# Kernel tuning notes

Measured on AMD Instinct MI355X. Metric: run time of the kernel, lower is better.

Reference implementation:

```python
import jax, jax.numpy as jnp
import numpy as np

N, E, IN_DIM, HID, G, NCLS, LAYERS = 200000, 1200000, 128, 64, 1024, 6, 3
BN_EPS = 1e-5


def _bn(x, g, b, m, v):
    # eval-mode BatchNorm1d with running stats
    return (x - m) * jax.lax.rsqrt(v + BN_EPS) * g + b


def setup_inputs() -> dict:
    key = jax.random.key(0)
    ks = jax.random.split(key, 24)
    s = 0.05
    d = {
        "x": jax.random.normal(ks[0], (N, IN_DIM), jnp.float32),
        "edge_index": jax.random.randint(ks[1], (2, E), 0, N, dtype=jnp.int32),
        "batch": jnp.sort(jax.random.randint(ks[2], (N,), 0, G, dtype=jnp.int32)),
        # input embedding + input BN
        "emb_w": jax.random.normal(ks[3], (IN_DIM, HID), jnp.float32) * s,
        "emb_b": jnp.zeros((HID,), jnp.float32),
        "ibn_g": jnp.ones((HID,), jnp.float32),
        "ibn_b": jnp.zeros((HID,), jnp.float32),
        "ibn_m": jax.random.normal(ks[4], (HID,), jnp.float32) * 0.1,
        "ibn_v": jax.random.uniform(ks[5], (HID,), jnp.float32, 0.5, 1.5),
        # stacked per-layer GIN MLP params [LAYERS, ...]
        "fc1_w": jax.random.normal(ks[6], (LAYERS, HID, HID), jnp.float32) * s,
        "fc1_b": jnp.zeros((LAYERS, HID), jnp.float32),
        "mbn_g": jnp.ones((LAYERS, HID), jnp.float32),
        "mbn_b": jnp.zeros((LAYERS, HID), jnp.float32),
        "mbn_m": jax.random.normal(ks[7], (LAYERS, HID), jnp.float32) * 0.1,
        "mbn_v": jax.random.uniform(ks[8], (LAYERS, HID), jnp.float32, 0.5, 1.5),
        "fc2_w": jax.random.normal(ks[9], (LAYERS, HID, HID), jnp.float32) * s,
        "fc2_b": jnp.zeros((LAYERS, HID), jnp.float32),
        # stacked per-layer outer BN params
        "obn_g": jnp.ones((LAYERS, HID), jnp.float32),
        "obn_b": jnp.zeros((LAYERS, HID), jnp.float32),
        "obn_m": jax.random.normal(ks[10], (LAYERS, HID), jnp.float32) * 0.1,
        "obn_v": jax.random.uniform(ks[11], (LAYERS, HID), jnp.float32, 0.5, 1.5),
        # classifier head
        "cls1_w": jax.random.normal(ks[12], (HID, HID // 2), jnp.float32) * s,
        "cls1_b": jnp.zeros((HID // 2,), jnp.float32),
        "cls2_w": jax.random.normal(ks[13], (HID // 2, NCLS), jnp.float32) * s,
        "cls2_b": jnp.zeros((NCLS,), jnp.float32),
    }
    return d


def reference(x, edge_index, batch,
              emb_w, emb_b, ibn_g, ibn_b, ibn_m, ibn_v,
              fc1_w, fc1_b, mbn_g, mbn_b, mbn_m, mbn_v, fc2_w, fc2_b,
              obn_g, obn_b, obn_m, obn_v,
              cls1_w, cls1_b, cls2_w, cls2_b):
    n = x.shape[0]
    src, dst = edge_index[0], edge_index[1]

    # input embed -> BN -> relu (dropout = identity in eval)
    h = jnp.dot(x, emb_w) + emb_b
    h = jax.nn.relu(_bn(h, ibn_g, ibn_b, ibn_m, ibn_v))

    for i in range(LAYERS):
        # GINConv (eps=0): aggregate neighbors via scatter-add, then MLP
        agg = jax.ops.segment_sum(h[src], dst, num_segments=n)
        z = h + agg
        z = jnp.dot(z, fc1_w[i]) + fc1_b[i]
        z = jax.nn.relu(_bn(z, mbn_g[i], mbn_b[i], mbn_m[i], mbn_v[i]))
        z = jnp.dot(z, fc2_w[i]) + fc2_b[i]
        # outer BN + relu
        h = jax.nn.relu(_bn(z, obn_g[i], obn_b[i], obn_m[i], obn_v[i]))

    # global mean pool per graph
    sums = jax.ops.segment_sum(h, batch, num_segments=G)
    cnts = jax.ops.segment_sum(jnp.ones((n,), h.dtype), batch, num_segments=G)
    pooled = sums / jnp.maximum(cnts, 1.0)[:, None]

    # classifier
    out = jax.nn.relu(jnp.dot(pooled, cls1_w) + cls1_b)
    out = jnp.dot(out, cls2_w) + cls2_b
    return out
```

## Files before the change

### kernel.cpp

```cpp
#include <hip/hip_runtime.h>
#include <hip/hip_bf16.h>

#define N_NODES 200000
#define N_EDGES 1200000
#define IN_DIM  128
#define HID     64
#define NGRAPH  1024
#define NCLS    6
#define BN_EPS  1e-5f

#define TILE_N   64
#define ZS       68
#define ECAP     1024

#define SCAN_CHUNK 1024
#define NBLK_SCAN ((N_NODES + SCAN_CHUNK - 1) / SCAN_CHUNK)

#define NBKT   128
#define BRANGE 1568
#define BCAP   12288
#define EPB    4096
#define NB_BIN ((N_EDGES + EPB - 1) / EPB)

typedef short bf16x8 __attribute__((ext_vector_type(8)));
typedef float f32x4  __attribute__((ext_vector_type(4)));
#define MFMA16(a,b,c) __builtin_amdgcn_mfma_f32_16x16x32_bf16((a),(b),(c),0,0,0)

__device__ __forceinline__ unsigned short f2bf(float f) {
    union { __hip_bfloat16 h; unsigned short u; } v; v.h = __float2bfloat16(f); return v.u;
}
__device__ __forceinline__ float bfbits2f(unsigned short u) {
    union { unsigned int i; float f; } v; v.i = ((unsigned int)u) << 16; return v.f;
}
__device__ __forceinline__ void cvt4(const float4& x, uint2& hi, uint2& lo) {
    const unsigned short h0 = f2bf(x.x), h1 = f2bf(x.y), h2 = f2bf(x.z), h3 = f2bf(x.w);
    hi.x = (unsigned)h0 | ((unsigned)h1 << 16);
    hi.y = (unsigned)h2 | ((unsigned)h3 << 16);
    const unsigned short l0 = f2bf(x.x - bfbits2f(h0)), l1 = f2bf(x.y - bfbits2f(h1));
    const unsigned short l2 = f2bf(x.z - bfbits2f(h2)), l3 = f2bf(x.w - bfbits2f(h3));
    lo.x = (unsigned)l0 | ((unsigned)l1 << 16);
    lo.y = (unsigned)l2 | ((unsigned)l3 << 16);
}

__global__ __launch_bounds__(256) void prep_emb_kernel(
    const float* __restrict__ w, unsigned short* __restrict__ wpe)
{
    const int idx = blockIdx.x * 256 + threadIdx.x;
    if (idx >= 16384) return;
    const int j = idx & 7, l = (idx >> 3) & 63;
    const int plane = (idx >> 9) & 1, s = (idx >> 10) & 3, ct = (idx >> 12) & 3;
    const int n = ct * 16 + (l & 15);
    const int k = s * 32 + (l >> 4) * 8 + j;
    const float f = w[k * 64 + n];
    const unsigned short hb = f2bf(f);
    wpe[idx] = plane ? f2bf(f - bfbits2f(hb)) : hb;
}

__global__ __launch_bounds__(256) void prep_fc_kernel(
    const float* __restrict__ fc1, const float* __restrict__ fc2,
    unsigned short* __restrict__ wpf)
{
    const int idx = blockIdx.x * 256 + threadIdx.x;
    if (idx >= 49152) return;
    const int j = idx & 7, l = (idx >> 3) & 63;
    const int plane = (idx >> 9) & 1, s = (idx >> 10) & 1, ct = (idx >> 11) & 3;
    const int g = (idx >> 13) & 1, layer = idx >> 14;
    const int n = ct * 16 + (l & 15);
    const int k = s * 32 + (l >> 4) * 8 + j;
    const float* W = g ? fc2 : fc1;
    const float f = W[(layer * 64 + k) * 64 + n];
    const unsigned short hb = f2bf(f);
    wpf[idx] = plane ? f2bf(f - bfbits2f(hb)) : hb;
}

__global__ __launch_bounds__(256) void bin_kernel(
    const int* __restrict__ src, const int* __restrict__ dst,
    int* __restrict__ gcnt, uint2* __restrict__ ebin)
{
    __shared__ int hist[NBKT];
    __shared__ int basis[NBKT];
    const int t = threadIdx.x;
    const int base = blockIdx.x * EPB;
    if (t < NBKT) hist[t] = 0;
    __syncthreads();
    int sv[16], dv[16];
    #pragma unroll
    for (int i = 0; i < 16; i++) {
        const int e = base + t + i * 256;
        if (e < N_EDGES) {
            sv[i] = src[e]; dv[i] = dst[e];
            atomicAdd(&hist[dv[i] / BRANGE], 1);
        } else { sv[i] = -1; dv[i] = -1; }
    }
    __syncthreads();
    if (t < NBKT) { basis[t] = atomicAdd(&gcnt[t], hist[t]); hist[t] = 0; }
    __syncthreads();
    #pragma unroll
    for (int i = 0; i < 16; i++) {
        if (dv[i] >= 0) {
            const int bb = dv[i] / BRANGE;
            const int pos = basis[bb] + atomicAdd(&hist[bb], 1);
            ebin[(size_t)bb * BCAP + pos] = make_uint2((unsigned)sv[i], (unsigned)dv[i]);
        }
    }
}

__global__ __launch_bounds__(512) void bindeg_kernel(
    const int* __restrict__ gcnt, const uint2* __restrict__ ebin,
    int* __restrict__ deg)
{
    __shared__ int hist[BRANGE];
    const int b = blockIdx.x, t = threadIdx.x;
    for (int i = t; i < BRANGE; i += 512) hist[i] = 0;
    __syncthreads();
    const int cnt = gcnt[b];
    const int r0 = b * BRANGE;
    const uint2* __restrict__ eb = ebin + (size_t)b * BCAP;
    for (int i = t; i < cnt; i += 512)
        atomicAdd(&hist[(int)eb[i].y - r0], 1);
    __syncthreads();
    for (int i = t; i < BRANGE; i += 512)
        if (r0 + i < N_NODES) deg[r0 + i] = hist[i];
}

__global__ __launch_bounds__(512) void binscatter_kernel(
    const int* __restrict__ gcnt, const uint2* __restrict__ ebin,
    const int* __restrict__ offs, int* __restrict__ csr_src)
{
    __shared__ int cur[BRANGE];
    const int b = blockIdx.x, t = threadIdx.x;
    const int r0 = b * BRANGE;
    const int lim = (r0 + BRANGE <= N_NODES) ? BRANGE : (N_NODES - r0);
    for (int i = t; i < lim; i += 512) cur[i] = offs[r0 + i];
    __syncthreads();
    const int cnt = gcnt[b];
    const uint2* __restrict__ eb = ebin + (size_t)b * BCAP;
    for (int i = t; i < cnt; i += 512) {
        const uint2 e = eb[i];
        const int pos = atomicAdd(&cur[(int)e.y - r0], 1);
        csr_src[pos] = (int)e.x;
    }
}

__global__ __launch_bounds__(256) void scan_sum_kernel(
    const int* __restrict__ deg, int* __restrict__ bsum)
{
    __shared__ int sd[256];
    const int b = blockIdx.x, t = threadIdx.x;
    const int base = b * SCAN_CHUNK;
    int s = 0;
    #pragma unroll
    for (int i = 0; i < SCAN_CHUNK / 256; i++) {
        const int idx = base + t + i * 256;
        s += (idx < N_NODES) ? deg[idx] : 0;
    }
    sd[t] = s; __syncthreads();
    for (int off = 128; off > 0; off >>= 1) {
        if (t < off) sd[t] += sd[t + off];
        __syncthreads();
    }
    if (t == 0) bsum[b] = sd[0];
}

__global__ __launch_bounds__(256) void scan_block_kernel(
    const int* __restrict__ bsum, int* __restrict__ boff, int* __restrict__ offs)
{
    __shared__ int sd[256];
    const int t = threadIdx.x;
    const int v = (t < NBLK_SCAN) ? bsum[t] : 0;
    sd[t] = v; __syncthreads();
    for (int off = 1; off < 256; off <<= 1) {
        const int u = (t >= off) ? sd[t - off] : 0;
        __syncthreads();
        sd[t] += u;
        __syncthreads();
    }
    if (t < NBLK_SCAN) boff[t] = sd[t] - v;
    if (t == 0) offs[N_NODES] = N_EDGES;
}

__global__ __launch_bounds__(256) void scan_scatter_kernel(
    const int* __restrict__ deg, const int* __restrict__ boff, int* __restrict__ offs)
{
    __shared__ int sd[256];
    const int b = blockIdx.x, t = threadIdx.x;
    const int base = b * SCAN_CHUNK + t * 4;
    int d0 = 0, d1 = 0, d2 = 0, d3 = 0;
    if (base + 0 < N_NODES) d0 = deg[base + 0];
    if (base + 1 < N_NODES) d1 = deg[base + 1];
    if (base + 2 < N_NODES) d2 = deg[base + 2];
    if (base + 3 < N_NODES) d3 = deg[base + 3];
    const int ts = d0 + d1 + d2 + d3;
    sd[t] = ts; __syncthreads();
    for (int off = 1; off < 256; off <<= 1) {
        const int u = (t >= off) ? sd[t - off] : 0;
        __syncthreads();
        sd[t] += u;
        __syncthreads();
    }
    const int excl = sd[t] - ts + boff[b];
    if (base + 0 < N_NODES) offs[base + 0] = excl;
    if (base + 1 < N_NODES) offs[base + 1] = excl + d0;
    if (base + 2 < N_NODES) offs[base + 2] = excl + d0 + d1;
    if (base + 3 < N_NODES) offs[base + 3] = excl + d0 + d1 + d2;
}

__global__ __launch_bounds__(256) void graph_offs_kernel(
    const int* __restrict__ batch, int* __restrict__ goffs)
{
    const int g = blockIdx.x * 256 + threadIdx.x;
    if (g > NGRAPH) return;
    if (g == NGRAPH) { goffs[NGRAPH] = N_NODES; return; }
    int lo = 0, hi = N_NODES;
    while (lo < hi) {
        const int mid = (lo + hi) >> 1;
        if (batch[mid] < g) lo = mid + 1; else hi = mid;
    }
    goffs[g] = lo;
}

__global__ __launch_bounds__(256) void pool_kernel(
    const float* __restrict__ h, const int* __restrict__ goffs,
    float* __restrict__ pooled, float* __restrict__ cnt)
{
    __shared__ float4 red[4][16];
    const int g = blockIdx.x, t = threadIdx.x;
    const int s = goffs[g], e = goffs[g + 1];
    const int grp = t >> 4;
    const int q = t & 15;
    float4 acc = {0.f, 0.f, 0.f, 0.f};
    for (int n = s + grp; n < e; n += 16) {
        const float4 v = *(const float4*)(h + (size_t)n * HID + q * 4);
        acc.x += v.x; acc.y += v.y; acc.z += v.z; acc.w += v.w;
    }
    #pragma unroll
    for (int off = 16; off <= 32; off <<= 1) {
        acc.x += __shfl_xor(acc.x, off, 64);
        acc.y += __shfl_xor(acc.y, off, 64);
        acc.z += __shfl_xor(acc.z, off, 64);
        acc.w += __shfl_xor(acc.w, off, 64);
    }
    const int wv = t >> 6, lane = t & 63;
    if (lane < 16) red[wv][lane] = acc;
    __syncthreads();
    if (t < 16) {
        float4 a = red[0][t];
        const float4 b = red[1][t], c = red[2][t], d = red[3][t];
        a.x += b.x + c.x + d.x;
        a.y += b.y + c.y + d.y;
        a.z += b.z + c.z + d.z;
        a.w += b.w + c.w + d.w;
        *(float4*)(pooled + (size_t)g * HID + t * 4) = a;
    }
    if (t == 0) cnt[g] = (float)(e - s);
}

__global__ __launch_bounds__(256) void embed_kernel(
    const float* __restrict__ x, const unsigned short* __restrict__ wpe,
    const float* __restrict__ bias,
    const float* __restrict__ bn_g, const float* __restrict__ bn_b,
    const float* __restrict__ bn_m, const float* __restrict__ bn_v,
    float* __restrict__ h)
{
    __shared__ __align__(16) short Abuf[4 * 4 * 2 * 64 * 8];
    __shared__ float Ztmp[TILE_N * ZS];
    __shared__ float BNs[128];
    const int t = threadIdx.x, lane = t & 63, w = t >> 6;
    const int base = blockIdx.x * TILE_N;

    if (t < 64) {
        const float s = bn_g[t] * rsqrtf(bn_v[t] + BN_EPS);
        BNs[t] = s;
        BNs[64 + t] = bias[t] * s + bn_b[t] - bn_m[t] * s;
    }
    #pragma unroll
    for (int i = 0; i < 8; i++) {
        const int idx = t + i * 256;
        const int n = idx >> 5, k4 = idx & 31;
        const float4 v = *(const float4*)(x + (size_t)(base + n) * IN_DIM + k4 * 4);
        uint2 hi, lo; cvt4(v, hi, lo);
        const int s = k4 >> 3, lc = (n & 15) + 16 * ((k4 >> 1) & 3);
        const int half = k4 & 1, wm = n >> 4;
        *(uint2*)&Abuf[(((wm * 4 + s) * 2 + 0) * 64 + lc) * 8 + half * 4] = hi;
        *(uint2*)&Abuf[(((wm * 4 + s) * 2 + 1) * 64 + lc) * 8 + half * 4] = lo;
    }
    __syncthreads();

    const bf16x8* A = (const bf16x8*)Abuf;
    const bf16x8* B = (const bf16x8*)wpe;
    bf16x8 ah[4], al[4];
    #pragma unroll
    for (int s = 0; s < 4; s++) {
        ah[s] = A[((w * 4 + s) * 2 + 0) * 64 + lane];
        al[s] = A[((w * 4 + s) * 2 + 1) * 64 + lane];
    }
    const int q = lane >> 4, c = lane & 15;
    #pragma unroll
    for (int ct = 0; ct < 4; ct++) {
        f32x4 acc = {0.f, 0.f, 0.f, 0.f};
        #pragma unroll
        for (int s = 0; s < 4; s++) {
            const bf16x8 bh = B[(ct << 9) + (s << 7) + lane];
            const bf16x8 bl = B[(ct << 9) + (s << 7) + 64 + lane];
            acc = MFMA16(ah[s], bh, acc);
            acc = MFMA16(ah[s], bl, acc);
            acc = MFMA16(al[s], bh, acc);
        }
        const int n = ct * 16 + c;
        const float sc = BNs[n], sh = BNs[64 + n];
        #pragma unroll
        for (int r = 0; r < 4; r++)
            Ztmp[(w * 16 + q * 4 + r) * ZS + n] = fmaxf(acc[r] * sc + sh, 0.f);
    }
    __syncthreads();
    #pragma unroll
    for (int i = 0; i < 4; i++) {
        const int idx = t + i * 256, n = idx >> 4, k4 = idx & 15;
        *(float4*)(h + (size_t)(base + n) * HID + k4 * 4) =
            *(const float4*)(&Ztmp[n * ZS + k4 * 4]);
    }
}

__global__ __launch_bounds__(256) void agg_mlp_kernel(
    const float* __restrict__ hin, float* __restrict__ hout,
    const int* __restrict__ offs, const int* __restrict__ csr,
    const unsigned short* __restrict__ wp1, const unsigned short* __restrict__ wp2,
    const float* __restrict__ b1, const float* __restrict__ g1,
    const float* __restrict__ bb1, const float* __restrict__ m1, const float* __restrict__ v1,
    const float* __restrict__ b2, const float* __restrict__ g2,
    const float* __restrict__ bb2, const float* __restrict__ m2, const float* __restrict__ v2)
{
    __shared__ __align__(16) short Abuf[4 * 2 * 2 * 64 * 8];
    __shared__ float Ztmp[TILE_N * ZS];
    __shared__ int   OF[TILE_N + 1];
    __shared__ int   EIDX[ECAP];
    __shared__ float BNs[256];
    const int t = threadIdx.x, lane = t & 63, w = t >> 6;
    const int sub = lane >> 4, cq = lane & 15;
    const int base = blockIdx.x * TILE_N;

    if (t < 64) {
        const float sa = g1[t] * rsqrtf(v1[t] + BN_EPS);
        BNs[t] = sa; BNs[64 + t] = b1[t] * sa + bb1[t] - m1[t] * sa;
        const float sb = g2[t] * rsqrtf(v2[t] + BN_EPS);
        BNs[128 + t] = sb; BNs[192 + t] = b2[t] * sb + bb2[t] - m2[t] * sb;
    }
    if (t <= TILE_N) OF[t] = offs[base + t];
    const int segStart = offs[base];
    const int segEnd   = offs[base + TILE_N];
    for (int i = t; i < segEnd - segStart; i += 256)
        if (i < ECAP) EIDX[i] = csr[segStart + i];
    __syncthreads();

    const float* __restrict__ hc = hin + cq * 4;
    #pragma unroll
    for (int p = 0; p < 4; p++) {
        const int mloc = p * 4 + sub, nl = w * 16 + mloc;
        const int e0 = OF[nl], e1 = OF[nl + 1];
        float4 acc = *(const float4*)(hin + (size_t)(base + nl) * HID + cq * 4);
        if (e0 < e1) {
            const int e1m = e1 - 1;
            for (int e = e0; e < e1; e += 4) {
                const int ea = e;
                const int eb = (e + 1 < e1) ? e + 1 : e1m;
                const int ec = (e + 2 < e1) ? e + 2 : e1m;
                const int ed = (e + 3 < e1) ? e + 3 : e1m;
                const int la = ea - segStart, lb = eb - segStart;
                const int lc2 = ec - segStart, ld = ed - segStart;
                const int s0 = (la < ECAP) ? EIDX[la] : csr[ea];
                const int s1 = (lb < ECAP) ? EIDX[lb] : csr[eb];
                const int s2 = (lc2 < ECAP) ? EIDX[lc2] : csr[ec];
                const int s3 = (ld < ECAP) ? EIDX[ld] : csr[ed];
                const float4 v0 = *(const float4*)(hc + (size_t)s0 * HID);
                const float4 v1_ = *(const float4*)(hc + (size_t)s1 * HID);
                const float4 v2_ = *(const float4*)(hc + (size_t)s2 * HID);
                const float4 v3_ = *(const float4*)(hc + (size_t)s3 * HID);
                const float mk1 = (e + 1 < e1) ? 1.f : 0.f;
                const float mk2 = (e + 2 < e1) ? 1.f : 0.f;
                const float mk3 = (e + 3 < e1) ? 1.f : 0.f;
                acc.x += v0.x + mk1 * v1_.x + mk2 * v2_.x + mk3 * v3_.x;
                acc.y += v0.y + mk1 * v1_.y + mk2 * v2_.y + mk3 * v3_.y;
                acc.z += v0.z + mk1 * v1_.z + mk2 * v2_.z + mk3 * v3_.z;
                acc.w += v0.w + mk1 * v1_.w + mk2 * v2_.w + mk3 * v3_.w;
            }
        }
        uint2 hi, lo; cvt4(acc, hi, lo);
        const int s = cq >> 3, lc = mloc + 16 * ((cq >> 1) & 3), half = cq & 1;
        *(uint2*)&Abuf[(((w * 2 + s) * 2 + 0) * 64 + lc) * 8 + half * 4] = hi;
        *(uint2*)&Abuf[(((w * 2 + s) * 2 + 1) * 64 + lc) * 8 + half * 4] = lo;
    }
    __syncthreads();

    const bf16x8* A = (const bf16x8*)Abuf;
    const int q = lane >> 4, c = lane & 15;

    {
        const bf16x8 a0h = A[((w * 2 + 0) * 2 + 0) * 64 + lane];
        const bf16x8 a0l = A[((w * 2 + 0) * 2 + 1) * 64 + lane];
        const bf16x8 a1h = A[((w * 2 + 1) * 2 + 0) * 64 + lane];
        const bf16x8 a1l = A[((w * 2 + 1) * 2 + 1) * 64 + lane];
        const bf16x8* B = (const bf16x8*)wp1;
        #pragma unroll
        for (int ct = 0; ct < 4; ct++) {
            const bf16x8 b0h = B[(ct << 8) + lane];
            const bf16x8 b0l = B[(ct << 8) + 64 + lane];
            const bf16x8 b1h_ = B[(ct << 8) + 128 + lane];
            const bf16x8 b1l_ = B[(ct << 8) + 192 + lane];
            f32x4 acc = {0.f, 0.f, 0.f, 0.f};
            acc = MFMA16(a0h, b0h, acc);
            acc = MFMA16(a0h, b0l, acc);
            acc = MFMA16(a0l, b0h, acc);
            acc = MFMA16(a1h, b1h_, acc);
            acc = MFMA16(a1h, b1l_, acc);
            acc = MFMA16(a1l, b1h_, acc);
            const int n = ct * 16 + c;
            const float sc = BNs[n], sh = BNs[64 + n];
            #pragma unroll
            for (int r = 0; r < 4; r++)
                Ztmp[(w * 16 + q * 4 + r) * ZS + n] = fmaxf(acc[r] * sc + sh, 0.f);
        }
    }
    __syncthreads();

    {
        const int m = t >> 2;
        #pragma unroll
        for (int d = 0; d < 4; d++) {
            const int k4 = (t & 3) * 4 + d;
            const float4 v = *(const float4*)(&Ztmp[m * ZS + k4 * 4]);
            uint2 hi, lo; cvt4(v, hi, lo);
            const int s = k4 >> 3, lc = (m & 15) + 16 * ((k4 >> 1) & 3);
            const int half = k4 & 1, wm = m >> 4;
            *(uint2*)&Abuf[(((wm * 2 + s) * 2 + 0) * 64 + lc) * 8 + half * 4] = hi;
            *(uint2*)&Abuf[(((wm * 2 + s) * 2 + 1) * 64 + lc) * 8 + half * 4] = lo;
        }
    }
    __syncthreads();

    {
        const bf16x8 a0h = A[((w * 2 + 0) * 2 + 0) * 64 + lane];
        const bf16x8 a0l = A[((w * 2 + 0) * 2 + 1) * 64 + lane];
        const bf16x8 a1h = A[((w * 2 + 1) * 2 + 0) * 64 + lane];
        const bf16x8 a1l = A[((w * 2 + 1) * 2 + 1) * 64 + lane];
        const bf16x8* B = (const bf16x8*)wp2;
        #pragma unroll
        for (int ct = 0; ct < 4; ct++) {
            const bf16x8 b0h = B[(ct << 8) + lane];
            const bf16x8 b0l = B[(ct << 8) + 64 + lane];
            const bf16x8 b1h_ = B[(ct << 8) + 128 + lane];
            const bf16x8 b1l_ = B[(ct << 8) + 192 + lane];
            f32x4 acc = {0.f, 0.f, 0.f, 0.f};
            acc = MFMA16(a0h, b0h, acc);
            acc = MFMA16(a0h, b0l, acc);
            acc = MFMA16(a0l, b0h, acc);
            acc = MFMA16(a1h, b1h_, acc);
            acc = MFMA16(a1h, b1l_, acc);
            acc = MFMA16(a1l, b1h_, acc);
            const int n = ct * 16 + c;
            const float sc = BNs[128 + n], sh = BNs[192 + n];
            #pragma unroll
            for (int r = 0; r < 4; r++)
                Ztmp[(w * 16 + q * 4 + r) * ZS + n] = fmaxf(acc[r] * sc + sh, 0.f);
        }
    }
    __syncthreads();

    #pragma unroll
    for (int i = 0; i < 4; i++) {
        const int idx = t + i * 256, n = idx >> 4, k4 = idx & 15;
        *(float4*)(hout + (size_t)(base + n) * HID + k4 * 4) =
            *(const float4*)(&Ztmp[n * ZS + k4 * 4]);
    }
}

__global__ __launch_bounds__(64) void cls_kernel(
    const float* __restrict__ pooled, const float* __restrict__ cnt,
    const float* __restrict__ w1, const float* __restrict__ b1,
    const float* __restrict__ w2, const float* __restrict__ b2,
    float* __restrict__ out)
{
    const int g = blockIdx.x;
    const int lane = threadIdx.x;
    const float c = cnt[g];
    const float p = pooled[(size_t)g * HID + lane] / fmaxf(c, 1.f);
    float acc = (lane < 32) ? b1[lane] : 0.f;
    #pragma unroll
    for (int k = 0; k < 64; k++) {
        const float pk = __shfl(p, k, 64);
        if (lane < 32) acc += pk * w1[k * 32 + lane];
    }
    const float hmid = fmaxf(acc, 0.f);
    float acc2 = (lane < NCLS) ? b2[lane] : 0.f;
    #pragma unroll
    for (int k = 0; k < 32; k++) {
        const float hk = __shfl(hmid, k, 64);
        if (lane < NCLS) acc2 += hk * w2[k * NCLS + lane];
    }
    if (lane < NCLS) out[(size_t)g * NCLS + lane] = acc2;
}

extern "C" void kernel_launch(void* const* d_in, const int* in_sizes, int n_in,
                              void* d_out, int out_size, void* d_ws, size_t ws_size,
                              hipStream_t stream) {
    const float* x     = (const float*)d_in[0];
    const int*   ei    = (const int*)d_in[1];
    const int*   batch = (const int*)d_in[2];
    const float* emb_w = (const float*)d_in[3];
    const float* emb_b = (const float*)d_in[4];
    const float* ibn_g = (const float*)d_in[5];
    const float* ibn_b = (const float*)d_in[6];
    const float* ibn_m = (const float*)d_in[7];
    const float* ibn_v = (const float*)d_in[8];
    const float* fc1_w = (const float*)d_in[9];
    const float* fc1_b = (const float*)d_in[10];
    const float* mbn_g = (const float*)d_in[11];
    const float* mbn_b = (const float*)d_in[12];
    const float* mbn_m = (const float*)d_in[13];
    const float* mbn_v = (const float*)d_in[14];
    const float* fc2_w = (const float*)d_in[15];
    const float* fc2_b = (const float*)d_in[16];
    const float* obn_g = (const float*)d_in[17];
    const float* obn_b = (const float*)d_in[18];
    const float* obn_m = (const float*)d_in[19];
    const float* obn_v = (const float*)d_in[20];
    const float* cls1w = (const float*)d_in[21];
    const float* cls1b = (const float*)d_in[22];
    const float* cls2w = (const float*)d_in[23];
    const float* cls2b = (const float*)d_in[24];

    float* h0     = (float*)d_ws;
    float* h1     = h0 + (size_t)N_NODES * HID;
    float* pooled = h1 + (size_t)N_NODES * HID;
    float* cnt    = pooled + NGRAPH * HID;
    int*   deg    = (int*)(cnt + NGRAPH);
    int*   offs   = deg + N_NODES;
    int*   bsum   = offs + (N_NODES + 1);
    int*   boff   = bsum + NBLK_SCAN;
    int*   csr    = boff + NBLK_SCAN;
    unsigned short* wpe = (unsigned short*)(csr + N_EDGES);
    unsigned short* wpf = wpe + 16384;
    int*   goffs  = (int*)(wpf + 49152);
    int*   gcnt   = goffs + (NGRAPH + 1);
    uint2* ebin   = (uint2*)h0;

    const int* src = ei;
    const int* dst = ei + N_EDGES;

    prep_emb_kernel<<<64, 256, 0, stream>>>(emb_w, wpe);
    prep_fc_kernel<<<192, 256, 0, stream>>>(fc1_w, fc2_w, wpf);

    graph_offs_kernel<<<(NGRAPH + 256) / 256, 256, 0, stream>>>(batch, goffs);

    hipMemsetAsync(gcnt, 0, NBKT * sizeof(int), stream);
    bin_kernel<<<NB_BIN, 256, 0, stream>>>(src, dst, gcnt, ebin);
    bindeg_kernel<<<NBKT, 512, 0, stream>>>(gcnt, ebin, deg);
    scan_sum_kernel<<<NBLK_SCAN, 256, 0, stream>>>(deg, bsum);
    scan_block_kernel<<<1, 256, 0, stream>>>(bsum, boff, offs);
    scan_scatter_kernel<<<NBLK_SCAN, 256, 0, stream>>>(deg, boff, offs);
    binscatter_kernel<<<NBKT, 512, 0, stream>>>(gcnt, ebin, offs, csr);

    const int gemm_blocks = N_NODES / TILE_N;
    embed_kernel<<<gemm_blocks, 256, 0, stream>>>(x, wpe, emb_b,
                                                  ibn_g, ibn_b, ibn_m, ibn_v, h0);

    const float* hin = h0;
    float* hout = h1;
    for (int i = 0; i < 3; i++) {
        agg_mlp_kernel<<<gemm_blocks, 256, 0, stream>>>(
            hin, hout, offs, csr,
            wpf + (size_t)(i * 2 + 0) * 8192, wpf + (size_t)(i * 2 + 1) * 8192,
            fc1_b + i * HID, mbn_g + i * HID, mbn_b + i * HID, mbn_m + i * HID, mbn_v + i * HID,
            fc2_b + i * HID, obn_g + i * HID, obn_b + i * HID, obn_m + i * HID, obn_v + i * HID);
        const float* tmp = hin; hin = hout; hout = (float*)tmp;
    }

    pool_kernel<<<NGRAPH, 256, 0, stream>>>(h1, goffs, pooled, cnt);

    cls_kernel<<<NGRAPH, 64, 0, stream>>>(pooled, cnt, cls1w, cls1b, cls2w, cls2b,
                                          (float*)d_out);
}
```

Measured before the change: 526.9 us.

## Alias A-fragment and Z staging buffers in LDS, swizzle slots, raise occupancy

The bf16 A-fragment buffer and the fp32 Ztmp staging tile now share one LDS allocation in both the embed and agg/MLP kernels, with extra barriers so each phase finishes reading before the next overwrites it. An XOR swizzle is applied to the 16-byte fragment slot index to spread LDS bank accesses. agg_mlp_kernel gets a launch_bounds occupancy hint of 7 blocks. The aim is lower LDS use and more resident blocks for the latency-bound gather, at the cost of additional __syncthreads and possible register-pressure spills.

```diff
diff --git a/kernel.cpp b/kernel.cpp
--- a/kernel.cpp
+++ b/kernel.cpp
@@ -21,6 +21,8 @@
 #define BCAP   12288
 #define EPB    4096
 #define NB_BIN ((N_EDGES + EPB - 1) / EPB)
+
+#define SWZ(s) ((s) ^ (((s) >> 4) & 3))
 
 typedef short bf16x8 __attribute__((ext_vector_type(8)));
 typedef float f32x4  __attribute__((ext_vector_type(4)));
@@ -262,9 +264,10 @@
     const float* __restrict__ bn_m, const float* __restrict__ bn_v,
     float* __restrict__ h)
 {
-    __shared__ __align__(16) short Abuf[4 * 4 * 2 * 64 * 8];
-    __shared__ float Ztmp[TILE_N * ZS];
+    __shared__ __align__(16) float Ush[8192];
     __shared__ float BNs[128];
+    short* Abuf = (short*)Ush;
+    float* Ztmp = Ush;
     const int t = threadIdx.x, lane = t & 63, w = t >> 6;
     const int base = blockIdx.x * TILE_N;
 
@@ -281,8 +284,10 @@
         uint2 hi, lo; cvt4(v, hi, lo);
         const int s = k4 >> 3, lc = (n & 15) + 16 * ((k4 >> 1) & 3);
         const int half = k4 & 1, wm = n >> 4;
-        *(uint2*)&Abuf[(((wm * 4 + s) * 2 + 0) * 64 + lc) * 8 + half * 4] = hi;
-        *(uint2*)&Abuf[(((wm * 4 + s) * 2 + 1) * 64 + lc) * 8 + half * 4] = lo;
+        const int sl0 = ((wm * 4 + s) * 2 + 0) * 64 + lc;
+        const int sl1 = ((wm * 4 + s) * 2 + 1) * 64 + lc;
+        *(uint2*)&Abuf[SWZ(sl0) * 8 + half * 4] = hi;
+        *(uint2*)&Abuf[SWZ(sl1) * 8 + half * 4] = lo;
     }
     __syncthreads();
 
@@ -291,9 +296,10 @@
     bf16x8 ah[4], al[4];
     #pragma unroll
     for (int s = 0; s < 4; s++) {
-        ah[s] = A[((w * 4 + s) * 2 + 0) * 64 + lane];
-        al[s] = A[((w * 4 + s) * 2 + 1) * 64 + lane];
-    }
+        ah[s] = A[SWZ(((w * 4 + s) * 2 + 0) * 64 + lane)];
+        al[s] = A[SWZ(((w * 4 + s) * 2 + 1) * 64 + lane)];
+    }
+    __syncthreads();
     const int q = lane >> 4, c = lane & 15;
     #pragma unroll
     for (int ct = 0; ct < 4; ct++) {
@@ -321,7 +327,7 @@
     }
 }
 
-__global__ __launch_bounds__(256) void agg_mlp_kernel(
+__global__ __launch_bounds__(256, 7) void agg_mlp_kernel(
     const float* __restrict__ hin, float* __restrict__ hout,
     const int* __restrict__ offs, const int* __restrict__ csr,
     const unsigned short* __restrict__ wp1, const unsigned short* __restrict__ wp2,
@@ -330,11 +336,12 @@
     const float* __restrict__ b2, const float* __restrict__ g2,
     const float* __restrict__ bb2, const float* __restrict__ m2, const float* __restrict__ v2)
 {
-    __shared__ __align__(16) short Abuf[4 * 2 * 2 * 64 * 8];
-    __shared__ float Ztmp[TILE_N * ZS];
+    __shared__ __align__(16) float Ush[TILE_N * ZS];
     __shared__ int   OF[TILE_N + 1];
     __shared__ int   EIDX[ECAP];
     __shared__ float BNs[256];
+    short* Abuf = (short*)Ush;
+    float* Ztmp = Ush;
     const int t = threadIdx.x, lane = t & 63, w = t >> 6;
     const int sub = lane >> 4, cq = lane & 15;
     const int base = blockIdx.x * TILE_N;
@@ -386,8 +393,10 @@
         }
         uint2 hi, lo; cvt4(acc, hi, lo);
         const int s = cq >> 3, lc = mloc + 16 * ((cq >> 1) & 3), half = cq & 1;
-        *(uint2*)&Abuf[(((w * 2 + s) * 2 + 0) * 64 + lc) * 8 + half * 4] = hi;
-        *(uint2*)&Abuf[(((w * 2 + s) * 2 + 1) * 64 + lc) * 8 + half * 4] = lo;
+        const int sl0 = ((w * 2 + s) * 2 + 0) * 64 + lc;
+        const int sl1 = ((w * 2 + s) * 2 + 1) * 64 + lc;
+        *(uint2*)&Abuf[SWZ(sl0) * 8 + half * 4] = hi;
+        *(uint2*)&Abuf[SWZ(sl1) * 8 + half * 4] = lo;
     }
     __syncthreads();
 
@@ -395,10 +404,11 @@
     const int q = lane >> 4, c = lane & 15;
 
     {
-        const bf16x8 a0h = A[((w * 2 + 0) * 2 + 0) * 64 + lane];
-        const bf16x8 a0l = A[((w * 2 + 0) * 2 + 1) * 64 + lane];
-        const bf16x8 a1h = A[((w * 2 + 1) * 2 + 0) * 64 + lane];
-        const bf16x8 a1l = A[((w * 2 + 1) * 2 + 1) * 64 + lane];
+        const bf16x8 a0h = A[SWZ(((w * 2 + 0) * 2 + 0) * 64 + lane)];
+        const bf16x8 a0l = A[SWZ(((w * 2 + 0) * 2 + 1) * 64 + lane)];
+        const bf16x8 a1h = A[SWZ(((w * 2 + 1) * 2 + 0) * 64 + lane)];
+        const bf16x8 a1l = A[SWZ(((w * 2 + 1) * 2 + 1) * 64 + lane)];
+        __syncthreads();
         const bf16x8* B = (const bf16x8*)wp1;
         #pragma unroll
         for (int ct = 0; ct < 4; ct++) {
@@ -424,24 +434,33 @@
 
     {
         const int m = t >> 2;
+        float4 vv[4];
         #pragma unroll
         for (int d = 0; d < 4; d++) {
             const int k4 = (t & 3) * 4 + d;
-            const float4 v = *(const float4*)(&Ztmp[m * ZS + k4 * 4]);
-            uint2 hi, lo; cvt4(v, hi, lo);
+            vv[d] = *(const float4*)(&Ztmp[m * ZS + k4 * 4]);
+        }
+        __syncthreads();
+        #pragma unroll
+        for (int d = 0; d < 4; d++) {
+            const int k4 = (t & 3) * 4 + d;
+            uint2 hi, lo; cvt4(vv[d], hi, lo);
             const int s = k4 >> 3, lc = (m & 15) + 16 * ((k4 >> 1) & 3);
             const int half = k4 & 1, wm = m >> 4;
-            *(uint2*)&Abuf[(((wm * 2 + s) * 2 + 0) * 64 + lc) * 8 + half * 4] = hi;
-            *(uint2*)&Abuf[(((wm * 2 + s) * 2 + 1) * 64 + lc) * 8 + half * 4] = lo;
+            const int sl0 = ((wm * 2 + s) * 2 + 0) * 64 + lc;
+            const int sl1 = ((wm * 2 + s) * 2 + 1) * 64 + lc;
+            *(uint2*)&Abuf[SWZ(sl0) * 8 + half * 4] = hi;
+            *(uint2*)&Abuf[SWZ(sl1) * 8 + half * 4] = lo;
         }
     }
     __syncthreads();
 
     {
-        const bf16x8 a0h = A[((w * 2 + 0) * 2 + 0) * 64 + lane];
-        const bf16x8 a0l = A[((w * 2 + 0) * 2 + 1) * 64 + lane];
-        const bf16x8 a1h = A[((w * 2 + 1) * 2 + 0) * 64 + lane];
-        const bf16x8 a1l = A[((w * 2 + 1) * 2 + 1) * 64 + lane];
+        const bf16x8 a0h = A[SWZ(((w * 2 + 0) * 2 + 0) * 64 + lane)];
+        const bf16x8 a0l = A[SWZ(((w * 2 + 0) * 2 + 1) * 64 + lane)];
+        const bf16x8 a1h = A[SWZ(((w * 2 + 1) * 2 + 0) * 64 + lane)];
+        const bf16x8 a1l = A[SWZ(((w * 2 + 1) * 2 + 1) * 64 + lane)];
+        __syncthreads();
         const bf16x8* B = (const bf16x8*)wp2;
         #pragma unroll
         for (int ct = 0; ct < 4; ct++) {
```

Result: faster. 497.9 us (-5.5%).
